# Optimization experiments

Hardware: AMD Instinct MI355X
Metric: run time of the kernel (lower is better)

## Reference

```python
import jax, jax.numpy as jnp
import numpy as np

B, C, T = 4, 1024, 2048
H = 16            # num_heads
G = 32            # GroupNorm groups (normalization(channels) == GroupNorm(32, C))
EPS = 1e-5


def setup_inputs() -> dict:
    key = jax.random.key(0)
    ks = jax.random.split(key, 7)
    x = jax.random.normal(ks[0], (B, C, T), dtype=jnp.float32)
    gn_scale = jax.random.normal(ks[1], (C,), dtype=jnp.float32) * 0.02 + 1.0
    gn_bias = jax.random.normal(ks[2], (C,), dtype=jnp.float32) * 0.02
    qkv_w = jax.random.normal(ks[3], (3 * C, C), dtype=jnp.float32) / np.sqrt(C)
    qkv_b = jax.random.normal(ks[4], (3 * C,), dtype=jnp.float32) * 0.02
    # NOTE: original zero-inits proj_out; randomized here so output != x for testing.
    proj_w = jax.random.normal(ks[5], (C, C), dtype=jnp.float32) / np.sqrt(C)
    proj_b = jax.random.normal(ks[6], (C,), dtype=jnp.float32) * 0.02
    return {"x": x, "gn_scale": gn_scale, "gn_bias": gn_bias,
            "qkv_w": qkv_w, "qkv_b": qkv_b, "proj_w": proj_w, "proj_b": proj_b}


def reference(x, gn_scale, gn_bias, qkv_w, qkv_b, proj_w, proj_b):
    b, c, t = x.shape
    ch = c // H
    # GroupNorm(32, C) over (channels-in-group, T)
    xg = x.reshape(b, G, c // G, t)
    mean = xg.mean(axis=(2, 3), keepdims=True)
    var = xg.var(axis=(2, 3), keepdims=True)
    xn = ((xg - mean) * jax.lax.rsqrt(var + EPS)).reshape(b, c, t)
    xn = xn * gn_scale[None, :, None] + gn_bias[None, :, None]
    # 1x1 conv QKV: [B, 3C, T]
    qkv = jnp.einsum('oc,bct->bot', qkv_w, xn) + qkv_b[None, :, None]
    q, k, v = jnp.split(qkv, 3, axis=1)
    # split heads -> [B*H, ch, T]
    q = q.reshape(b * H, ch, t)
    k = k.reshape(b * H, ch, t)
    v = v.reshape(b * H, ch, t)
    scale = 1.0 / np.sqrt(np.sqrt(ch)).astype(np.float32)
    # full T x T attention weights, softmax in fp32 (as original)
    w = jnp.einsum('bct,bcs->bts', q * scale, k * scale)
    w = jax.nn.softmax(w.astype(jnp.float32), axis=-1).astype(w.dtype)
    a = jnp.einsum('bts,bcs->bct', w, v).reshape(b, c, t)
    # 1x1 conv projection + residual
    h = jnp.einsum('oc,bct->bot', proj_w, a) + proj_b[None, :, None]
    return x + h
```

## Files before the change

kernel.cpp:

```cpp
#include <hip/hip_runtime.h>
#include <hip/hip_bf16.h>
#include <stdint.h>

#define Bn 4
#define Cn 1024
#define Tn 2048
#define Hn 16
#define Gn 32
#define SCALE_Q 0.18033688f

typedef short short8  __attribute__((ext_vector_type(8)));
typedef short short4_t __attribute__((ext_vector_type(4)));
typedef float float4_t __attribute__((ext_vector_type(4)));
typedef unsigned int uint2_t __attribute__((ext_vector_type(2)));

__device__ __forceinline__ short f2bf(float f) {
    uint32_t u = __float_as_uint(f);
    uint32_t r = (u + 0x7FFFu + ((u >> 16) & 1u)) >> 16;
    return (short)r;
}

__device__ __forceinline__ float exp2_fast(float x) {
#if __has_builtin(__builtin_amdgcn_exp2f)
    return __builtin_amdgcn_exp2f(x);
#else
    return exp2f(x);
#endif
}

__device__ __forceinline__ uint32_t pack_bf16_trunc(float lo, float hi) {
#if __has_builtin(__builtin_amdgcn_perm)
    return __builtin_amdgcn_perm(__float_as_uint(hi), __float_as_uint(lo), 0x07060302u);
#else
    return (__float_as_uint(lo) >> 16) | (__float_as_uint(hi) & 0xFFFF0000u);
#endif
}

__device__ __forceinline__ void permswap32(uint32_t& x, uint32_t& y) {
#if __has_builtin(__builtin_amdgcn_permlane32_swap)
    uint2_t r = __builtin_amdgcn_permlane32_swap(x, y, false, false);
    x = r[0]; y = r[1];
#else
    asm volatile("v_permlane32_swap_b32 %0, %1" : "+v"(x), "+v"(y));
#endif
}
__device__ __forceinline__ void permswap16(uint32_t& x, uint32_t& y) {
#if __has_builtin(__builtin_amdgcn_permlane16_swap)
    uint2_t r = __builtin_amdgcn_permlane16_swap(x, y, false, false);
    x = r[0]; y = r[1];
#else
    asm volatile("v_permlane16_swap_b32 %0, %1" : "+v"(x), "+v"(y));
#endif
}

#define GLL16(gptr, lptr)                                                      \
    __builtin_amdgcn_global_load_lds(                                          \
        (const __attribute__((address_space(1))) unsigned int*)(gptr),         \
        (__attribute__((address_space(3))) unsigned int*)(lptr), 16, 0, 0)

__global__ __launch_bounds__(256) void cvt_w2(const float* __restrict__ srcA,
                                              const float* __restrict__ srcB,
                                              short* __restrict__ dst) {
    int i = blockIdx.x * 256 + threadIdx.x;
    float4_t v = (i < 786432)
        ? reinterpret_cast<const float4_t*>(srcA)[i]
        : reinterpret_cast<const float4_t*>(srcB)[i - 786432];
    short4_t o;
    o[0] = f2bf(v[0]); o[1] = f2bf(v[1]); o[2] = f2bf(v[2]); o[3] = f2bf(v[3]);
    reinterpret_cast<short4_t*>(dst)[i] = o;
}

__global__ __launch_bounds__(256) void gn_stats(const float* __restrict__ x,
                                                float* __restrict__ part) {
    int lin = blockIdx.x;
    int sl = lin & 7, g = (lin >> 3) & 31, b = lin >> 8;
    const float4_t* base = reinterpret_cast<const float4_t*>(
        x + ((size_t)(b * Cn + g * 32)) * Tn) + sl * 2048;
    int tid = threadIdx.x;
    float s = 0.f, ss = 0.f;
    #pragma unroll
    for (int k = 0; k < 8; k++) {
        float4_t v = base[tid + k * 256];
        s  += v[0] + v[1] + v[2] + v[3];
        ss += v[0]*v[0] + v[1]*v[1] + v[2]*v[2] + v[3]*v[3];
    }
    #pragma unroll
    for (int m = 1; m < 64; m <<= 1) { s += __shfl_xor(s, m); ss += __shfl_xor(ss, m); }
    __shared__ float red[8];
    int wave = tid >> 6;
    if ((tid & 63) == 0) { red[wave * 2] = s; red[wave * 2 + 1] = ss; }
    __syncthreads();
    if (tid == 0) {
        part[lin * 2]     = red[0] + red[2] + red[4] + red[6];
        part[lin * 2 + 1] = red[1] + red[3] + red[5] + red[7];
    }
}

__global__ __launch_bounds__(256) void gn_apply(const float* __restrict__ x,
                                                const float* __restrict__ gs,
                                                const float* __restrict__ gb,
                                                const float* __restrict__ part,
                                                short* __restrict__ xnT) {
    int lin = blockIdx.x;
    int sl = lin & 7, g = (lin >> 3) & 31, b = lin >> 8;
    const float* base = x + ((size_t)(b * Cn + g * 32)) * Tn;
    int tid = threadIdx.x;
    int pb = (lin >> 3) << 3;
    float ts = 0.f, tss = 0.f;
    #pragma unroll
    for (int i = 0; i < 8; i++) {
        ts  += part[(pb + i) * 2];
        tss += part[(pb + i) * 2 + 1];
    }
    float mean = ts * (1.f / 65536.f);
    float var  = tss * (1.f / 65536.f) - mean * mean;
    float rstd = rsqrtf(var + 1e-5f);

    __shared__ float tile[64][33];
    int tbase = sl * 256;
    for (int t0 = tbase; t0 < tbase + 256; t0 += 64) {
        #pragma unroll
        for (int k = 0; k < 8; k++) {
            int e = tid + k * 256;
            int c = e >> 6, tt = e & 63;
            float v = base[c * Tn + t0 + tt];
            tile[tt][c] = (v - mean) * rstd * gs[g * 32 + c] + gb[g * 32 + c];
        }
        __syncthreads();
        #pragma unroll
        for (int k = 0; k < 8; k++) {
            int f = tid + k * 256;
            int tt = f >> 5, c = f & 31;
            xnT[((size_t)(b * Tn + t0 + tt)) * Cn + g * 32 + c] = f2bf(tile[tt][c]);
        }
        __syncthreads();
    }
}

__global__ __launch_bounds__(512, 2) void gemm256_k(const short* __restrict__ W,
                                                    const short* __restrict__ Bm,
                                                    const float* __restrict__ bias,
                                                    short* __restrict__ qkT,
                                                    short* __restrict__ vbuf) {
    constexpr int K = 1024;
    constexpr int NT = K / 64;
    __shared__ short As[2][256 * 64];
    __shared__ short Bs[2][256 * 64];

    int m0 = blockIdx.x * 256, n0 = blockIdx.y * 256, b = blockIdx.z;
    int tid = threadIdx.x;
    int wave = tid >> 6, lane = tid & 63, quad = lane >> 4, l15 = lane & 15;
    int wm = wave >> 2, wn = wave & 3;
    const short* Ab = W + (size_t)m0 * K;
    const short* Bb = Bm + ((size_t)b * Tn + n0) * K;

    float4_t acc[8][4];
    float4_t z = {0.f, 0.f, 0.f, 0.f};
    #pragma unroll
    for (int i = 0; i < 8; i++)
        #pragma unroll
        for (int j = 0; j < 4; j++) acc[i][j] = z;

    int sw = l15 & 7;

    auto stage = [&](int buf, int k0) {
        #pragma unroll
        for (int r = 0; r < 4; r++) {
            int cid = r * 512 + tid;
            int row = cid >> 3, j = cid & 7;
            int ch = j ^ (row & 7);
            GLL16(Ab + (size_t)row * K + k0 + ch * 8, &As[buf][cid * 8]);
            GLL16(Bb + (size_t)row * K + k0 + ch * 8, &Bs[buf][cid * 8]);
        }
    };

    stage(0, 0);
    stage(1, 64);
    __builtin_amdgcn_sched_barrier(0);
    asm volatile("s_waitcnt vmcnt(8)" ::: "memory");
    __builtin_amdgcn_sched_barrier(0);
    __builtin_amdgcn_s_barrier();
    __builtin_amdgcn_sched_barrier(0);

    for (int it = 0; it < NT; ++it) {
        int cur = it & 1;
        #pragma unroll
        for (int kk = 0; kk < 2; kk++) {
            short8 af[8], bfg[4];
            #pragma unroll
            for (int mi = 0; mi < 8; mi++)
                af[mi] = *reinterpret_cast<const short8*>(
                    &As[cur][(wm * 128 + mi * 16 + l15) * 64 + ((4 * kk + quad) ^ sw) * 8]);
            #pragma unroll
            for (int ni = 0; ni < 4; ni++)
                bfg[ni] = *reinterpret_cast<const short8*>(
                    &Bs[cur][(wn * 64 + ni * 16 + l15) * 64 + ((4 * kk + quad) ^ sw) * 8]);
            #pragma unroll
            for (int mi = 0; mi < 8; mi++)
                #pragma unroll
                for (int ni = 0; ni < 4; ni++)
                    acc[mi][ni] = __builtin_amdgcn_mfma_f32_16x16x32_bf16(
                        af[mi], bfg[ni], acc[mi][ni], 0, 0, 0);
        }
        __builtin_amdgcn_sched_barrier(0);
        __builtin_amdgcn_s_barrier();
        __builtin_amdgcn_sched_barrier(0);
        if (it + 2 < NT) stage(cur, (it + 2) * 64);
        __builtin_amdgcn_sched_barrier(0);
        if (it + 2 < NT) {
            asm volatile("s_waitcnt vmcnt(8)" ::: "memory");
        } else if (it + 1 < NT) {
            asm volatile("s_waitcnt vmcnt(0)" ::: "memory");
        }
        __builtin_amdgcn_sched_barrier(0);
        __builtin_amdgcn_s_barrier();
        __builtin_amdgcn_sched_barrier(0);
    }

    #pragma unroll
    for (int mi = 0; mi < 8; mi++) {
        int mrow = m0 + wm * 128 + mi * 16 + quad * 4;
        #pragma unroll
        for (int ni = 0; ni < 4; ni++) {
            int t = n0 + wn * 64 + ni * 16 + l15;
            if (mrow < 2048) {
                int hh = mrow >> 6, ch = mrow & 63;
                float sc = (mrow < 1024) ? SCALE_Q : 1.0f;
                short4_t pk;
                #pragma unroll
                for (int r = 0; r < 4; r++)
                    pk[r] = f2bf((acc[mi][ni][r] + bias[mrow + r]) * sc);
                *reinterpret_cast<short4_t*>(
                    &qkT[(((size_t)b * 32 + hh) * Tn + t) * 64 + ch]) = pk;
            } else {
                int c = mrow - 2048;
                #pragma unroll
                for (int r = 0; r < 4; r++)
                    vbuf[((size_t)b * Cn + c + r) * Tn + t] =
                        f2bf(acc[mi][ni][r] + bias[mrow + r]);
            }
        }
    }
}

__global__ __launch_bounds__(256) void gemm_k(const short* __restrict__ W,
                                              const short* __restrict__ Bm,
                                              const float* __restrict__ bias,
                                              const float* __restrict__ xres,
                                              float* __restrict__ outp) {
    constexpr int K = 1024;
    constexpr int NT = K / 64;
    __shared__ short As[2][128 * 64];
    __shared__ short Bs[2][128 * 64];

    int m0 = blockIdx.x * 128, n0 = blockIdx.y * 128, b = blockIdx.z;
    int tid = threadIdx.x;
    int wave = tid >> 6, lane = tid & 63, quad = lane >> 4, l15 = lane & 15;
    int wm = wave >> 1, wn = wave & 1;
    const short* Ab = W + (size_t)m0 * K;
    const short* Bb = Bm + ((size_t)b * Tn + n0) * K;

    float4_t acc[4][4];
    float4_t z = {0.f, 0.f, 0.f, 0.f};
    #pragma unroll
    for (int i = 0; i < 4; i++)
        #pragma unroll
        for (int j = 0; j < 4; j++) acc[i][j] = z;

    int sw = l15 & 7;

    auto stage = [&](int buf, int k0) {
        #pragma unroll
        for (int r = 0; r < 4; r++) {
            int cid = r * 256 + tid;
            int row = cid >> 3, j = cid & 7;
            int ch = j ^ (row & 7);
            GLL16(Ab + (size_t)row * K + k0 + ch * 8, &As[buf][cid * 8]);
            GLL16(Bb + (size_t)row * K + k0 + ch * 8, &Bs[buf][cid * 8]);
        }
    };

    stage(0, 0);
    stage(1, 64);
    __builtin_amdgcn_sched_barrier(0);
    asm volatile("s_waitcnt vmcnt(8)" ::: "memory");
    __builtin_amdgcn_sched_barrier(0);
    __builtin_amdgcn_s_barrier();
    __builtin_amdgcn_sched_barrier(0);

    for (int it = 0; it < NT; ++it) {
        int cur = it & 1;
        #pragma unroll
        for (int kk = 0; kk < 2; kk++) {
            short8 af[4], bfg[4];
            #pragma unroll
            for (int mi = 0; mi < 4; mi++)
                af[mi] = *reinterpret_cast<const short8*>(
                    &As[cur][(wm * 64 + mi * 16 + l15) * 64 + ((4 * kk + quad) ^ sw) * 8]);
            #pragma unroll
            for (int ni = 0; ni < 4; ni++)
                bfg[ni] = *reinterpret_cast<const short8*>(
                    &Bs[cur][(wn * 64 + ni * 16 + l15) * 64 + ((4 * kk + quad) ^ sw) * 8]);
            #pragma unroll
            for (int mi = 0; mi < 4; mi++)
                #pragma unroll
                for (int ni = 0; ni < 4; ni++)
                    acc[mi][ni] = __builtin_amdgcn_mfma_f32_16x16x32_bf16(
                        af[mi], bfg[ni], acc[mi][ni], 0, 0, 0);
        }
        __builtin_amdgcn_sched_barrier(0);
        __builtin_amdgcn_s_barrier();
        __builtin_amdgcn_sched_barrier(0);
        if (it + 2 < NT) stage(cur, (it + 2) * 64);
        __builtin_amdgcn_sched_barrier(0);
        if (it + 2 < NT) {
            asm volatile("s_waitcnt vmcnt(8)" ::: "memory");
        } else if (it + 1 < NT) {
            asm volatile("s_waitcnt vmcnt(0)" ::: "memory");
        }
        __builtin_amdgcn_sched_barrier(0);
        __builtin_amdgcn_s_barrier();
        __builtin_amdgcn_sched_barrier(0);
    }

    #pragma unroll
    for (int mi = 0; mi < 4; mi++) {
        int mrow = m0 + wm * 64 + mi * 16 + quad * 4;
        #pragma unroll
        for (int ni = 0; ni < 4; ni++) {
            int t = n0 + wn * 64 + ni * 16 + l15;
            #pragma unroll
            for (int r = 0; r < 4; r++) {
                size_t idx = ((size_t)b * Cn + mrow + r) * Tn + t;
                outp[idx] = xres[idx] + bias[mrow + r] + acc[mi][ni][r];
            }
        }
    }
}

__global__ __launch_bounds__(512, 4) void attn_k(const short* __restrict__ qkT,
                                                 const short* __restrict__ vbuf,
                                                 short* __restrict__ aT) {
    __shared__ short ks[2][64 * 72];
    __shared__ short vs[2][64 * 72];
    int bh = blockIdx.y; int b = bh >> 4, h = bh & 15;
    int t0 = blockIdx.x * 256;
    int tid = threadIdx.x;
    int wave = tid >> 6, lane = tid & 63, quad = lane >> 4, l15 = lane & 15;
    const short* qb = qkT + (((size_t)b * 32 + h) * Tn) * 64;
    const short* kb = qkT + (((size_t)b * 32 + 16 + h) * Tn) * 64;
    const short* vb = vbuf + ((size_t)b * Cn + h * 64) * Tn;
    int tw = t0 + wave * 32;

    short8 qf[2][2];
    #pragma unroll
    for (int tni = 0; tni < 2; tni++)
        #pragma unroll
        for (int kk = 0; kk < 2; kk++)
            qf[tni][kk] = *reinterpret_cast<const short8*>(
                qb + ((size_t)(tw + tni * 16 + l15)) * 64 + kk * 32 + quad * 8);

    short8 ones;
    #pragma unroll
    for (int i = 0; i < 8; i++) ones[i] = (short)0x3F80;

    float4_t z = {0.f, 0.f, 0.f, 0.f};
    float4_t acc[2][4], lacc[2];
    #pragma unroll
    for (int i = 0; i < 2; i++) {
        lacc[i] = z;
        #pragma unroll
        for (int j = 0; j < 4; j++) acc[i][j] = z;
    }

    int srow = tid >> 3, soff = (tid & 7) * 8;
    const short* kgp = kb + (size_t)srow * 64 + soff;
    const short* vgp = vb + (size_t)srow * Tn + soff;
    short* krd = &ks[0][0]; short* kwr = &ks[1][0];
    short* vrd = &vs[0][0]; short* vwr = &vs[1][0];
    int sdst = srow * 72 + soff;

    {
        uint4 k0v = *reinterpret_cast<const uint4*>(kgp);
        uint4 v0v = *reinterpret_cast<const uint4*>(vgp);
        *reinterpret_cast<uint4*>(&krd[sdst]) = k0v;
        *reinterpret_cast<uint4*>(&vrd[sdst]) = v0v;
    }
    __syncthreads();

    for (int it = 0; it < Tn / 64; ++it) {
        uint4 knx, vnx;
        if (it < Tn / 64 - 1) {
            knx = *reinterpret_cast<const uint4*>(kgp + (size_t)(it + 1) * 64 * 64);
            vnx = *reinterpret_cast<const uint4*>(vgp + (size_t)(it + 1) * 64);
        }

        #pragma unroll
        for (int pr = 0; pr < 2; pr++) {
            uint32_t pk[2][2][2];
            #pragma unroll
            for (int half = 0; half < 2; half++) {
                int smi = pr * 2 + half;
                float4_t sa[2] = {z, z};
                __builtin_amdgcn_s_setprio(1);
                #pragma unroll
                for (int kk = 0; kk < 2; kk++) {
                    short8 kf = *reinterpret_cast<const short8*>(
                        &krd[(smi * 16 + l15) * 72 + kk * 32 + quad * 8]);
                    #pragma unroll
                    for (int tni = 0; tni < 2; tni++)
                        sa[tni] = __builtin_amdgcn_mfma_f32_16x16x32_bf16(
                            kf, qf[tni][kk], sa[tni], 0, 0, 0);
                }
                __builtin_amdgcn_s_setprio(0);
                #pragma unroll
                for (int tni = 0; tni < 2; tni++) {
                    float p0 = exp2_fast(sa[tni][0]);
                    float p1 = exp2_fast(sa[tni][1]);
                    float p2 = exp2_fast(sa[tni][2]);
                    float p3 = exp2_fast(sa[tni][3]);
                    pk[half][tni][0] = pack_bf16_trunc(p0, p1);
                    pk[half][tni][1] = pack_bf16_trunc(p2, p3);
                }
            }
            short8 vf[4];
            #pragma unroll
            for (int ci = 0; ci < 4; ci++)
                vf[ci] = *reinterpret_cast<const short8*>(
                    &vrd[(ci * 16 + l15) * 72 + pr * 32 + quad * 8]);
            #pragma unroll
            for (int tni = 0; tni < 2; tni++) {
                uint32_t x0 = pk[0][tni][0], y0 = pk[1][tni][0];
                permswap32(x0, y0); permswap16(x0, y0);
                uint32_t x1 = pk[0][tni][1], y1 = pk[1][tni][1];
                permswap32(x1, y1); permswap16(x1, y1);
                uint4 afu = {x0, x1, y0, y1};
                short8 af = *reinterpret_cast<short8*>(&afu);
                __builtin_amdgcn_s_setprio(1);
                lacc[tni] = __builtin_amdgcn_mfma_f32_16x16x32_bf16(
                    af, ones, lacc[tni], 0, 0, 0);
                #pragma unroll
                for (int ci = 0; ci < 4; ci++)
                    acc[tni][ci] = __builtin_amdgcn_mfma_f32_16x16x32_bf16(
                        af, vf[ci], acc[tni][ci], 0, 0, 0);
                __builtin_amdgcn_s_setprio(0);
            }
        }

        if (it < Tn / 64 - 1) {
            *reinterpret_cast<uint4*>(&kwr[sdst]) = knx;
            *reinterpret_cast<uint4*>(&vwr[sdst]) = vnx;
        }
        __syncthreads();
        short* tk = krd; krd = kwr; kwr = tk;
        short* tv = vrd; vrd = vwr; vwr = tv;
    }

    #pragma unroll
    for (int tni = 0; tni < 2; tni++) {
        #pragma unroll
        for (int r = 0; r < 4; r++) {
            float rl = 1.0f / lacc[tni][r];
            int t = tw + tni * 16 + quad * 4 + r;
            #pragma unroll
            for (int ci = 0; ci < 4; ci++) {
                int ch = ci * 16 + l15;
                aT[((size_t)b * Tn + t) * Cn + h * 64 + ch] =
                    f2bf(acc[tni][ci][r] * rl);
            }
        }
    }
}

extern "C" void kernel_launch(void* const* d_in, const int* in_sizes, int n_in,
                              void* d_out, int out_size, void* d_ws, size_t ws_size,
                              hipStream_t stream) {
    const float* x     = (const float*)d_in[0];
    const float* gs    = (const float*)d_in[1];
    const float* gb    = (const float*)d_in[2];
    const float* qkvw  = (const float*)d_in[3];
    const float* qkvb  = (const float*)d_in[4];
    const float* projw = (const float*)d_in[5];
    const float* projb = (const float*)d_in[6];
    float* out = (float*)d_out;

    char* ws = (char*)d_ws;
    short* wqkv  = (short*)(ws + 0);
    short* wproj = (short*)(ws + 6291456);
    short* xnT   = (short*)(ws + 8388608);
    short* aT    = (short*)(ws + 8388608);
    short* qkT   = (short*)(ws + 25165824);
    float* gnp   = (float*)(ws + 25165824);
    short* vbuf  = (short*)(ws + 58720256);

    cvt_w2<<<dim3(4096), dim3(256), 0, stream>>>(qkvw, projw, wqkv);
    gn_stats<<<dim3(1024), dim3(256), 0, stream>>>(x, gnp);
    gn_apply<<<dim3(1024), dim3(256), 0, stream>>>(x, gs, gb, gnp, xnT);
    gemm256_k<<<dim3(12, 8, 4), dim3(512), 0, stream>>>(wqkv, xnT, qkvb,
                                                        qkT, vbuf);
    attn_k<<<dim3(8, 64), dim3(512), 0, stream>>>(qkT, vbuf, aT);
    gemm_k<<<dim3(8, 16, 4), dim3(256), 0, stream>>>(wproj, aT, projb, x, out);
}
```

Measured before the change: 287.5 us.

## Shrink QKV GEMM tiles to 128x128x32 with a triple-buffered LDS pipeline

The QKV projection GEMM moves from 256x256 tiles with BK=64, 512 threads and double buffering to 128x128 tiles with BK=32, 256 threads and a three-stage LDS ring. The prefetch is now issued before compute, and each iteration needs one barrier instead of two. The grid grows from 384 to 1536 blocks, which gives better occupancy and wave balance across the CUs. The cost is less data reuse per tile, so the kernel does more global and LDS traffic per FLOP.

```diff
diff --git a/kernel.cpp b/kernel.cpp
--- a/kernel.cpp
+++ b/kernel.cpp
@@ -137,89 +137,91 @@
     }
 }
 
-__global__ __launch_bounds__(512, 2) void gemm256_k(const short* __restrict__ W,
-                                                    const short* __restrict__ Bm,
-                                                    const float* __restrict__ bias,
-                                                    short* __restrict__ qkT,
-                                                    short* __restrict__ vbuf) {
+__global__ __launch_bounds__(256, 3) void gemm_qkv(const short* __restrict__ W,
+                                                   const short* __restrict__ Bm,
+                                                   const float* __restrict__ bias,
+                                                   short* __restrict__ qkT,
+                                                   short* __restrict__ vbuf) {
     constexpr int K = 1024;
-    constexpr int NT = K / 64;
-    __shared__ short As[2][256 * 64];
-    __shared__ short Bs[2][256 * 64];
-
-    int m0 = blockIdx.x * 256, n0 = blockIdx.y * 256, b = blockIdx.z;
+    constexpr int BK = 32;
+    constexpr int NT = K / BK;
+    __shared__ short As[3][128 * BK];
+    __shared__ short Bs[3][128 * BK];
+
+    int m0 = blockIdx.x * 128, n0 = blockIdx.y * 128, b = blockIdx.z;
     int tid = threadIdx.x;
     int wave = tid >> 6, lane = tid & 63, quad = lane >> 4, l15 = lane & 15;
-    int wm = wave >> 2, wn = wave & 3;
+    int wm = wave >> 1, wn = wave & 1;
     const short* Ab = W + (size_t)m0 * K;
     const short* Bb = Bm + ((size_t)b * Tn + n0) * K;
 
-    float4_t acc[8][4];
+    float4_t acc[4][4];
     float4_t z = {0.f, 0.f, 0.f, 0.f};
     #pragma unroll
-    for (int i = 0; i < 8; i++)
+    for (int i = 0; i < 4; i++)
         #pragma unroll
         for (int j = 0; j < 4; j++) acc[i][j] = z;
 
-    int sw = l15 & 7;
+    int sw = (l15 >> 1) & 3;
 
     auto stage = [&](int buf, int k0) {
         #pragma unroll
-        for (int r = 0; r < 4; r++) {
-            int cid = r * 512 + tid;
-            int row = cid >> 3, j = cid & 7;
-            int ch = j ^ (row & 7);
+        for (int r = 0; r < 2; r++) {
+            int cid = r * 256 + tid;
+            int row = cid >> 2, j = cid & 3;
+            int ch = j ^ ((row >> 1) & 3);
             GLL16(Ab + (size_t)row * K + k0 + ch * 8, &As[buf][cid * 8]);
             GLL16(Bb + (size_t)row * K + k0 + ch * 8, &Bs[buf][cid * 8]);
         }
     };
 
     stage(0, 0);
-    stage(1, 64);
+    stage(1, BK);
     __builtin_amdgcn_sched_barrier(0);
-    asm volatile("s_waitcnt vmcnt(8)" ::: "memory");
+    asm volatile("s_waitcnt vmcnt(4)" ::: "memory");
     __builtin_amdgcn_sched_barrier(0);
     __builtin_amdgcn_s_barrier();
     __builtin_amdgcn_sched_barrier(0);
 
+    int cur = 0;
     for (int it = 0; it < NT; ++it) {
-        int cur = it & 1;
-        #pragma unroll
-        for (int kk = 0; kk < 2; kk++) {
-            short8 af[8], bfg[4];
-            #pragma unroll
-            for (int mi = 0; mi < 8; mi++)
+        if (it + 2 < NT) {
+            int nx = cur + 2; if (nx >= 3) nx -= 3;
+            stage(nx, (it + 2) * BK);
+        }
+        __builtin_amdgcn_sched_barrier(0);
+        {
+            short8 af[4], bfg[4];
+            #pragma unroll
+            for (int mi = 0; mi < 4; mi++)
                 af[mi] = *reinterpret_cast<const short8*>(
-                    &As[cur][(wm * 128 + mi * 16 + l15) * 64 + ((4 * kk + quad) ^ sw) * 8]);
+                    &As[cur][(wm * 64 + mi * 16 + l15) * BK + ((quad ^ sw) * 8)]);
             #pragma unroll
             for (int ni = 0; ni < 4; ni++)
                 bfg[ni] = *reinterpret_cast<const short8*>(
-                    &Bs[cur][(wn * 64 + ni * 16 + l15) * 64 + ((4 * kk + quad) ^ sw) * 8]);
-            #pragma unroll
-            for (int mi = 0; mi < 8; mi++)
+                    &Bs[cur][(wn * 64 + ni * 16 + l15) * BK + ((quad ^ sw) * 8)]);
+            #pragma unroll
+            for (int mi = 0; mi < 4; mi++)
                 #pragma unroll
                 for (int ni = 0; ni < 4; ni++)
                     acc[mi][ni] = __builtin_amdgcn_mfma_f32_16x16x32_bf16(
                         af[mi], bfg[ni], acc[mi][ni], 0, 0, 0);
         }
         __builtin_amdgcn_sched_barrier(0);
-        __builtin_amdgcn_s_barrier();
-        __builtin_amdgcn_sched_barrier(0);
-        if (it + 2 < NT) stage(cur, (it + 2) * 64);
-        __builtin_amdgcn_sched_barrier(0);
         if (it + 2 < NT) {
-            asm volatile("s_waitcnt vmcnt(8)" ::: "memory");
+            asm volatile("s_waitcnt vmcnt(4)" ::: "memory");
         } else if (it + 1 < NT) {
             asm volatile("s_waitcnt vmcnt(0)" ::: "memory");
         }
         __builtin_amdgcn_sched_barrier(0);
         __builtin_amdgcn_s_barrier();
         __builtin_amdgcn_sched_barrier(0);
-    }
-
-    #pragma unroll
-    for (int mi = 0; mi < 8; mi++) {
-        int mrow = m0 + wm * 128 + mi * 16 + quad * 4;
+        cur = (cur == 2) ? 0 : cur + 1;
+    }
+
+    #pragma unroll
+    for (int mi = 0; mi < 4; mi++) {
+        int mrow = m0 + wm * 64 + mi * 16 + quad * 4;
         #pragma unroll
         for (int ni = 0; ni < 4; ni++) {
             int t = n0 + wn * 64 + ni * 16 + l15;
@@ -496,7 +498,7 @@
     cvt_w2<<<dim3(4096), dim3(256), 0, stream>>>(qkvw, projw, wqkv);
     gn_stats<<<dim3(1024), dim3(256), 0, stream>>>(x, gnp);
     gn_apply<<<dim3(1024), dim3(256), 0, stream>>>(x, gs, gb, gnp, xnT);
-    gemm256_k<<<dim3(12, 8, 4), dim3(512), 0, stream>>>(wqkv, xnT, qkvb,
+    gemm_qkv<<<dim3(24, 16, 4), dim3(256), 0, stream>>>(wqkv, xnT, qkvb,
                                                         qkT, vbuf);
     attn_k<<<dim3(8, 64), dim3(512), 0, stream>>>(qkT, vbuf, aT);
     gemm_k<<<dim3(8, 16, 4), dim3(256), 0, stream>>>(wproj, aT, projb, x, out);
```

New measurement: 278.7 us. 1.03x faster.
